# Performance work log

Hardware: AMD Instinct MI355X
Metric: run time of the kernel (lower is better)

The kernel has to match this reference:

```python
import jax, jax.numpy as jnp
import numpy as np

N, E, F_IN, H, C, G = 100000, 1600000, 128, 128, 10, 64


def setup_inputs() -> dict:
    key = jax.random.key(0)
    ks = jax.random.split(key, 9)
    x = jax.random.normal(ks[0], (N, F_IN), dtype=jnp.float32)
    edge_index = jax.random.randint(ks[1], (2, E), 0, N, dtype=jnp.int32)
    batch = jnp.sort(jax.random.randint(ks[2], (N,), 0, G, dtype=jnp.int32))
    s_in = 1.0 / np.sqrt(F_IN)
    s_h = 1.0 / np.sqrt(H)
    W1 = jax.random.normal(ks[3], (F_IN, H), jnp.float32) * s_in
    b1 = jnp.zeros((H,), jnp.float32)
    W2 = jax.random.normal(ks[4], (H, H), jnp.float32) * s_h
    b2 = jnp.zeros((H,), jnp.float32)
    Wfc = jax.random.normal(ks[5], (H, C), jnp.float32) * s_h
    bfc = jnp.zeros((C,), jnp.float32)
    return {"x": x, "edge_index": edge_index, "batch": batch,
            "W1": W1, "b1": b1, "W2": W2, "b2": b2, "Wfc": Wfc, "bfc": bfc}


def _gcn_conv(x, W, b, src, dst, n):
    # GCNConv: xW, symmetric deg^-1/2 normalization with self-loops, scatter-add, +bias
    xw = x @ W  # [N, H]
    deg = jnp.zeros((n,), xw.dtype).at[dst].add(1.0)  # in-degree incl. self-loop
    dis = jax.lax.rsqrt(jnp.maximum(deg, 1.0))
    norm = dis[src] * dis[dst]  # [E+N]
    out = jnp.zeros_like(xw).at[dst].add(xw[src] * norm[:, None])
    return out + b


def reference(x, edge_index, batch, W1, b1, W2, b2, Wfc, bfc):
    n = x.shape[0]
    loop = jnp.arange(n, dtype=edge_index.dtype)  # self-loops
    src = jnp.concatenate([edge_index[0], loop])
    dst = jnp.concatenate([edge_index[1], loop])
    h = jax.nn.relu(_gcn_conv(x, W1, b1, src, dst, n))
    h = jax.nn.relu(_gcn_conv(h, W2, b2, src, dst, n))
    # global mean pool over graph ids
    sums = jax.ops.segment_sum(h, batch, num_segments=G)  # [G, H]
    cnt = jax.ops.segment_sum(jnp.ones((n, 1), h.dtype), batch, num_segments=G)
    pooled = sums / jnp.maximum(cnt, 1.0)
    return pooled @ Wfc + bfc  # [G, C]
```

## Files before the change

kernel.cpp:

```cpp
#include <hip/hip_runtime.h>
#include <hip/hip_bf16.h>

#define NN 100000
#define NE 1600000
#define HD 128
#define NG 64
#define NC 10
#define NB 391
#define BCAP 4608
#define CHUNK 6400
#define NBIN (NE / CHUNK)

typedef short bf16x8 __attribute__((ext_vector_type(8)));
typedef float f32x4 __attribute__((ext_vector_type(4)));

__device__ __forceinline__ unsigned pk_bf16(float a, float b) {
  unsigned ua = __float_as_uint(a);
  unsigned ub = __float_as_uint(b);
  unsigned ra = (ua + 0x7fffu + ((ua >> 16) & 1u)) >> 16;
  unsigned rb = (ub + 0x7fffu + ((ub >> 16) & 1u)) >> 16;
  return ra | (rb << 16);
}

#define ACC_U4(v)                                  \
  do {                                             \
    a0 += __uint_as_float((v).x << 16);            \
    a1 += __uint_as_float((v).x & 0xffff0000u);    \
    a2 += __uint_as_float((v).y << 16);            \
    a3 += __uint_as_float((v).y & 0xffff0000u);    \
    a4 += __uint_as_float((v).z << 16);            \
    a5 += __uint_as_float((v).z & 0xffff0000u);    \
    a6 += __uint_as_float((v).w << 16);            \
    a7 += __uint_as_float((v).w & 0xffff0000u);    \
  } while (0)

__global__ __launch_bounds__(256) void k_bin2(const int* __restrict__ src, const int* __restrict__ dst,
                                              int* __restrict__ bcnt, unsigned* __restrict__ bkt,
                                              const float* __restrict__ W1, const float* __restrict__ W2,
                                              unsigned* __restrict__ WT1, unsigned* __restrict__ WT2,
                                              const int* __restrict__ bat, int* __restrict__ sg,
                                              int* __restrict__ eg, float* __restrict__ sums) {
  __shared__ int cl[NB];
  __shared__ int cb[NB];
  int bid = blockIdx.x;
  int tid = threadIdx.x;
  if (bid >= NBIN) {
    int mb = bid - NBIN;
    if (mb < 64) {
      int i = mb * 256 + tid;
      const float* W = (i < 8192) ? W1 : W2;
      unsigned* WT = (i < 8192) ? WT1 : WT2;
      int j = i & 8191;
      int n = j >> 6, kh = j & 63;
      WT[j] = pk_bf16(W[(2 * kh) * HD + n], W[(2 * kh + 1) * HD + n]);
      if (i < NG * HD) sums[i] = 0.f;
    } else {
      int i = (mb - 64) * 256 + tid;
      if (i < NN) {
        int g = bat[i];
        if (i == 0 || bat[i - 1] != g) sg[g] = i;
        if (i == NN - 1 || bat[i + 1] != g) eg[g] = i + 1;
      }
    }
    return;
  }
  int base_e = bid * CHUNK;
  for (int i = tid; i < NB; i += 256) cl[i] = 0;
  __syncthreads();
  #pragma unroll 5
  for (int j = 0; j < CHUNK / 256; ++j) {
    int d = dst[base_e + j * 256 + tid];
    atomicAdd(&cl[d >> 8], 1);
  }
  __syncthreads();
  for (int i = tid; i < NB; i += 256) {
    cb[i] = atomicAdd(&bcnt[i], cl[i]);
    cl[i] = 0;
  }
  __syncthreads();
  #pragma unroll 5
  for (int j = 0; j < CHUNK / 256; ++j) {
    int e = base_e + j * 256 + tid;
    int s = src[e];
    int d = dst[e];
    int b = d >> 8;
    int p = atomicAdd(&cl[b], 1);
    int idx = cb[b] + p;
    if (idx < BCAP)
      bkt[(size_t)b * BCAP + idx] = (unsigned)s | ((unsigned)(d & 255) << 24);
  }
}

__global__ __launch_bounds__(256) void k_fill2(const unsigned* __restrict__ bkt,
                                               const int* __restrict__ bcnt,
                                               int* __restrict__ rows, int* __restrict__ rowe,
                                               float* __restrict__ dis, int* __restrict__ csr) {
  __shared__ unsigned eds[BCAP];
  __shared__ int sc[256];
  int b = blockIdx.x;
  int tid = threadIdx.x;
  int n = bcnt[b];
  if (n > BCAP) n = BCAP;
  const unsigned* mb = bkt + (size_t)b * BCAP;
  for (int i = tid; i < n; i += 256) eds[i] = mb[i];
  sc[tid] = 0;
  __syncthreads();
  for (int i = tid; i < n; i += 256) atomicAdd(&sc[eds[i] >> 24], 1);
  __syncthreads();
  int deg = sc[tid];
  for (int off = 1; off < 256; off <<= 1) {
    int v = (tid >= off) ? sc[tid - off] : 0;
    __syncthreads();
    sc[tid] += v;
    __syncthreads();
  }
  int excl = sc[tid] - deg;
  int node = b * 256 + tid;
  int cbase = b * BCAP;
  if (node < NN) {
    rows[node] = cbase + excl;
    rowe[node] = cbase + excl + deg;
    dis[node] = rsqrtf((float)(deg + 1));
  }
  __syncthreads();
  sc[tid] = excl;
  __syncthreads();
  for (int i = tid; i < n; i += 256) {
    unsigned v = eds[i];
    int p = atomicAdd(&sc[v >> 24], 1);
    csr[cbase + p] = (int)(v & 0xFFFFFFu);
  }
}

template<bool BF16IN>
__global__ __launch_bounds__(256) void k_gemm_mfma(const void* __restrict__ Xin,
                                                   const unsigned* __restrict__ WT,
                                                   const float* __restrict__ dis,
                                                   unsigned* __restrict__ Y) {
  __shared__ char WL[128 * 256];
  __shared__ char XL[64 * 256];
  int t = threadIdx.x;
  int rowBase = blockIdx.x * 64;
  {
    const uint4* Wg = (const uint4*)WT;
    for (int i = t; i < 2048; i += 256) {
      int n = i >> 4, kq = i & 15;
      uint4 v = Wg[i];
      *(uint4*)(WL + ((n * 256 + kq * 16) ^ ((n & 7) << 4))) = v;
    }
  }
  if (BF16IN) {
    const uint4* Xg = (const uint4*)Xin;
    for (int i = t; i < 1024; i += 256) {
      int node = i >> 4, c = i & 15;
      int gn = rowBase + node; if (gn >= NN) gn = 0;
      uint4 v = Xg[(size_t)gn * 16 + c];
      *(uint4*)(XL + ((node * 256 + c * 16) ^ ((node & 7) << 4))) = v;
    }
  } else {
    const float4* Xg = (const float4*)Xin;
    for (int i = t; i < 1024; i += 256) {
      int node = i >> 4, c = i & 15;
      int gn = rowBase + node; if (gn >= NN) gn = 0;
      float4 a = Xg[(size_t)gn * 32 + c * 2];
      float4 b = Xg[(size_t)gn * 32 + c * 2 + 1];
      uint4 v;
      v.x = pk_bf16(a.x, a.y); v.y = pk_bf16(a.z, a.w);
      v.z = pk_bf16(b.x, b.y); v.w = pk_bf16(b.z, b.w);
      *(uint4*)(XL + ((node * 256 + c * 16) ^ ((node & 7) << 4))) = v;
    }
  }
  __syncthreads();
  int w = t >> 6, l = t & 63;
  int lr = l & 15, lh = l >> 4;
  int xnode = w * 16 + lr;
  bf16x8 bfrag[4];
  #pragma unroll
  for (int ks = 0; ks < 4; ++ks)
    bfrag[ks] = *(bf16x8*)(XL + ((xnode * 256 + (ks * 32 + lh * 8) * 2) ^ ((xnode & 7) << 4)));
  f32x4 acc[8];
  #pragma unroll
  for (int ct = 0; ct < 8; ++ct) acc[ct] = (f32x4){0.f, 0.f, 0.f, 0.f};
  #pragma unroll
  for (int ct = 0; ct < 8; ++ct) {
    int n = ct * 16 + lr;
    #pragma unroll
    for (int ks = 0; ks < 4; ++ks) {
      bf16x8 af = *(bf16x8*)(WL + ((n * 256 + (ks * 32 + lh * 8) * 2) ^ ((n & 7) << 4)));
      acc[ct] = __builtin_amdgcn_mfma_f32_16x16x32_bf16(af, bfrag[ks], acc[ct], 0, 0, 0);
    }
  }
  int gnode = rowBase + w * 16 + lr;
  if (gnode < NN) {
    float ds = dis[gnode];
    uint2* Yp = (uint2*)(Y + (size_t)gnode * 64);
    #pragma unroll
    for (int ct = 0; ct < 8; ++ct) {
      uint2 o;
      o.x = pk_bf16(acc[ct].x * ds, acc[ct].y * ds);
      o.y = pk_bf16(acc[ct].z * ds, acc[ct].w * ds);
      Yp[ct * 4 + lh] = o;
    }
  }
}

__global__ __launch_bounds__(256) void k_agg(const unsigned* __restrict__ Y, const int* __restrict__ rows,
                                             const int* __restrict__ rowe, const int* __restrict__ csr,
                                             const float* __restrict__ dis,
                                             const float* __restrict__ bias,
                                             unsigned* __restrict__ OUT) {
  int node = __builtin_amdgcn_readfirstlane((blockIdx.x << 2) + (threadIdx.x >> 6));
  int lane = threadIdx.x & 63;
  int sub = lane >> 4, li = lane & 15;
  const uint4* Yv = (const uint4*)Y;
  float a0 = 0.f, a1 = 0.f, a2 = 0.f, a3 = 0.f, a4 = 0.f, a5 = 0.f, a6 = 0.f, a7 = 0.f;
  int start = rows[node], len = rowe[node] - start;
  if (sub == 0) {
    uint4 sv = Yv[(size_t)node * 16 + li];
    ACC_U4(sv);
  }
  int i = start + ((len * sub) >> 2);
  int q1 = start + ((len * (sub + 1)) >> 2);
  for (; i + 4 <= q1; i += 4) {
    int s0 = csr[i], s1 = csr[i + 1], s2 = csr[i + 2], s3 = csr[i + 3];
    uint4 v0 = Yv[(size_t)s0 * 16 + li];
    uint4 v1 = Yv[(size_t)s1 * 16 + li];
    uint4 v2 = Yv[(size_t)s2 * 16 + li];
    uint4 v3 = Yv[(size_t)s3 * 16 + li];
    ACC_U4(v0);
    ACC_U4(v1);
    ACC_U4(v2);
    ACC_U4(v3);
  }
  for (; i < q1; ++i) {
    uint4 v = Yv[(size_t)csr[i] * 16 + li];
    ACC_U4(v);
  }
  a0 += __shfl_xor(a0, 16, 64); a0 += __shfl_xor(a0, 32, 64);
  a1 += __shfl_xor(a1, 16, 64); a1 += __shfl_xor(a1, 32, 64);
  a2 += __shfl_xor(a2, 16, 64); a2 += __shfl_xor(a2, 32, 64);
  a3 += __shfl_xor(a3, 16, 64); a3 += __shfl_xor(a3, 32, 64);
  a4 += __shfl_xor(a4, 16, 64); a4 += __shfl_xor(a4, 32, 64);
  a5 += __shfl_xor(a5, 16, 64); a5 += __shfl_xor(a5, 32, 64);
  a6 += __shfl_xor(a6, 16, 64); a6 += __shfl_xor(a6, 32, 64);
  a7 += __shfl_xor(a7, 16, 64); a7 += __shfl_xor(a7, 32, 64);
  if (sub != 0) return;
  float di = dis[node];
  const float4* bp = (const float4*)bias;
  float4 b0 = bp[li * 2], b1 = bp[li * 2 + 1];
  float o0 = fmaxf(fmaf(di, a0, b0.x), 0.f);
  float o1 = fmaxf(fmaf(di, a1, b0.y), 0.f);
  float o2 = fmaxf(fmaf(di, a2, b0.z), 0.f);
  float o3 = fmaxf(fmaf(di, a3, b0.w), 0.f);
  float o4 = fmaxf(fmaf(di, a4, b1.x), 0.f);
  float o5 = fmaxf(fmaf(di, a5, b1.y), 0.f);
  float o6 = fmaxf(fmaf(di, a6, b1.z), 0.f);
  float o7 = fmaxf(fmaf(di, a7, b1.w), 0.f);
  uint4 pv;
  pv.x = pk_bf16(o0, o1);
  pv.y = pk_bf16(o2, o3);
  pv.z = pk_bf16(o4, o5);
  pv.w = pk_bf16(o6, o7);
  ((uint4*)OUT)[(size_t)node * 16 + li] = pv;
}

__global__ __launch_bounds__(256) void k_pool(const unsigned* __restrict__ Hb, const int* __restrict__ sg,
                                              const int* __restrict__ eg, float* __restrict__ sums) {
  int g = blockIdx.x >> 3;
  int sl = blockIdx.x & 7;
  int slot = threadIdx.x >> 6;
  int pl = threadIdx.x & 63;
  int s = sg[g], e = eg[g];
  float f0 = 0.f, f1 = 0.f;
  for (int n = s + sl * 4 + slot; n < e; n += 32) {
    unsigned v = Hb[(size_t)n * 64 + pl];
    f0 += __uint_as_float(v << 16);
    f1 += __uint_as_float(v & 0xffff0000u);
  }
  atomicAdd(&sums[g * HD + 2 * pl], f0);
  atomicAdd(&sums[g * HD + 2 * pl + 1], f1);
}

__global__ __launch_bounds__(640) void k_fc(const float* __restrict__ sums, const int* __restrict__ sg,
                                            const int* __restrict__ eg, const float* __restrict__ Wfc,
                                            const float* __restrict__ bfc, float* __restrict__ out) {
  int t = threadIdx.x;
  if (t >= NG * NC) return;
  int g = t / NC, c = t - g * NC;
  int cntn = eg[g] - sg[g];
  float inv = 1.0f / fmaxf((float)cntn, 1.0f);
  float acc = 0.f;
  for (int f = 0; f < HD; ++f) acc = fmaf(sums[g * HD + f], Wfc[f * NC + c], acc);
  out[t] = acc * inv + bfc[c];
}

extern "C" void kernel_launch(void* const* d_in, const int* in_sizes, int n_in,
                              void* d_out, int out_size, void* d_ws, size_t ws_size,
                              hipStream_t stream) {
  const float* x   = (const float*)d_in[0];
  const int*   ei  = (const int*)d_in[1];
  const int*   bat = (const int*)d_in[2];
  const float* W1  = (const float*)d_in[3];
  const float* b1  = (const float*)d_in[4];
  const float* W2  = (const float*)d_in[5];
  const float* b2  = (const float*)d_in[6];
  const float* Wfc = (const float*)d_in[7];
  const float* bfc = (const float*)d_in[8];
  float* out = (float*)d_out;
  const int* esrc = ei;
  const int* edst = ei + NE;

  char* p = (char*)d_ws;
  auto carve = [&](size_t bytes) { char* r = p; p += (bytes + 255) & ~(size_t)255; return r; };
  float* dis  = (float*)carve((size_t)NN * 4);
  int*   rows = (int*)carve((size_t)NN * 4);
  int*   rowe = (int*)carve((size_t)NN * 4);
  int*   bcnt = (int*)carve((size_t)NB * 4);
  int*   sg   = (int*)carve(NG * 4);
  int*   eg   = (int*)carve(NG * 4);
  float* sums = (float*)carve(NG * HD * 4);
  unsigned* WT1 = (unsigned*)carve(8192 * 4);
  unsigned* WT2 = (unsigned*)carve(8192 * 4);
  int*   csr  = (int*)carve((size_t)NB * BCAP * 4);
  unsigned* Y   = (unsigned*)carve((size_t)NN * 64 * 4);
  unsigned* H1b = (unsigned*)carve((size_t)NN * 64 * 4);
  unsigned* bkt = Y;
  unsigned* H2b = H1b;

  hipMemsetAsync(bcnt, 0, (size_t)NB * 4, stream);

  int miscBlocks = 64 + (NN + 255) / 256;
  k_bin2<<<NBIN + miscBlocks, 256, 0, stream>>>(esrc, edst, bcnt, bkt,
                                                W1, W2, WT1, WT2, bat, sg, eg, sums);
  k_fill2<<<NB, 256, 0, stream>>>(bkt, bcnt, rows, rowe, dis, csr);

  int gblocks = (NN + 63) / 64;
  k_gemm_mfma<false><<<gblocks, 256, 0, stream>>>(x, WT1, dis, Y);
  k_agg<<<NN / 4, 256, 0, stream>>>(Y, rows, rowe, csr, dis, b1, H1b);
  k_gemm_mfma<true><<<gblocks, 256, 0, stream>>>(H1b, WT2, dis, Y);
  k_agg<<<NN / 4, 256, 0, stream>>>(Y, rows, rowe, csr, dis, b2, H2b);

  k_pool<<<NG * 8, 256, 0, stream>>>(H2b, sg, eg, sums);
  k_fc<<<1, 640, 0, stream>>>(sums, sg, eg, Wfc, bfc, out);
}
```

Baseline: 248.9 us.

## Cache dst in registers, use wave-shuffle scan, double pool parallelism

The binning kernel now keeps each thread's dst values in registers from the counting pass, so the second pass does not reload them from global memory. The fill kernel replaces a 256-step shared-memory Hillis-Steele scan, which needed many barriers, with a 64-lane shuffle scan plus a small cross-wave fixup. The pooling kernel launches twice as many blocks per graph, giving more parallelism at the cost of more atomics. These are small preprocessing and tail-kernel tweaks and leave the dominant GEMM and aggregation kernels unchanged.

```diff
diff --git a/kernel.cpp b/kernel.cpp
--- a/kernel.cpp
+++ b/kernel.cpp
@@ -10,6 +10,7 @@
 #define BCAP 4608
 #define CHUNK 6400
 #define NBIN (NE / CHUNK)
+#define EPT (CHUNK / 256)
 
 typedef short bf16x8 __attribute__((ext_vector_type(8)));
 typedef float f32x4 __attribute__((ext_vector_type(4)));
@@ -65,11 +66,13 @@
     return;
   }
   int base_e = bid * CHUNK;
+  int dc[EPT];
   for (int i = tid; i < NB; i += 256) cl[i] = 0;
   __syncthreads();
-  #pragma unroll 5
-  for (int j = 0; j < CHUNK / 256; ++j) {
+  #pragma unroll
+  for (int j = 0; j < EPT; ++j) {
     int d = dst[base_e + j * 256 + tid];
+    dc[j] = d;
     atomicAdd(&cl[d >> 8], 1);
   }
   __syncthreads();
@@ -78,11 +81,10 @@
     cl[i] = 0;
   }
   __syncthreads();
-  #pragma unroll 5
-  for (int j = 0; j < CHUNK / 256; ++j) {
-    int e = base_e + j * 256 + tid;
-    int s = src[e];
-    int d = dst[e];
+  #pragma unroll
+  for (int j = 0; j < EPT; ++j) {
+    int s = src[base_e + j * 256 + tid];
+    int d = dc[j];
     int b = d >> 8;
     int p = atomicAdd(&cl[b], 1);
     int idx = cb[b] + p;
@@ -97,6 +99,7 @@
                                                float* __restrict__ dis, int* __restrict__ csr) {
   __shared__ unsigned eds[BCAP];
   __shared__ int sc[256];
+  __shared__ int wsum[4];
   int b = blockIdx.x;
   int tid = threadIdx.x;
   int n = bcnt[b];
@@ -108,13 +111,19 @@
   for (int i = tid; i < n; i += 256) atomicAdd(&sc[eds[i] >> 24], 1);
   __syncthreads();
   int deg = sc[tid];
-  for (int off = 1; off < 256; off <<= 1) {
-    int v = (tid >= off) ? sc[tid - off] : 0;
-    __syncthreads();
-    sc[tid] += v;
-    __syncthreads();
-  }
-  int excl = sc[tid] - deg;
+  int v = deg;
+  int lane = tid & 63;
+  #pragma unroll
+  for (int off = 1; off < 64; off <<= 1) {
+    int u = __shfl_up(v, off, 64);
+    if (lane >= off) v += u;
+  }
+  if (lane == 63) wsum[tid >> 6] = v;
+  __syncthreads();
+  int base = 0;
+  #pragma unroll
+  for (int w = 0; w < 4; ++w) base += (w < (tid >> 6)) ? wsum[w] : 0;
+  int excl = base + v - deg;
   int node = b * 256 + tid;
   int cbase = b * BCAP;
   if (node < NN) {
@@ -126,9 +135,9 @@
   sc[tid] = excl;
   __syncthreads();
   for (int i = tid; i < n; i += 256) {
-    unsigned v = eds[i];
-    int p = atomicAdd(&sc[v >> 24], 1);
-    csr[cbase + p] = (int)(v & 0xFFFFFFu);
+    unsigned v2 = eds[i];
+    int p = atomicAdd(&sc[v2 >> 24], 1);
+    csr[cbase + p] = (int)(v2 & 0xFFFFFFu);
   }
 }
 
@@ -266,13 +275,13 @@
 
 __global__ __launch_bounds__(256) void k_pool(const unsigned* __restrict__ Hb, const int* __restrict__ sg,
                                               const int* __restrict__ eg, float* __restrict__ sums) {
-  int g = blockIdx.x >> 3;
-  int sl = blockIdx.x & 7;
+  int g = blockIdx.x >> 4;
+  int sl = blockIdx.x & 15;
   int slot = threadIdx.x >> 6;
   int pl = threadIdx.x & 63;
   int s = sg[g], e = eg[g];
   float f0 = 0.f, f1 = 0.f;
-  for (int n = s + sl * 4 + slot; n < e; n += 32) {
+  for (int n = s + sl * 4 + slot; n < e; n += 64) {
     unsigned v = Hb[(size_t)n * 64 + pl];
     f0 += __uint_as_float(v << 16);
     f1 += __uint_as_float(v & 0xffff0000u);
@@ -340,6 +349,6 @@
   k_gemm_mfma<true><<<gblocks, 256, 0, stream>>>(H1b, WT2, dis, Y);
   k_agg<<<NN / 4, 256, 0, stream>>>(Y, rows, rowe, csr, dis, b2, H2b);
 
-  k_pool<<<NG * 8, 256, 0, stream>>>(H2b, sg, eg, sums);
+  k_pool<<<NG * 16, 256, 0, stream>>>(H2b, sg, eg, sums);
   k_fc<<<1, 640, 0, stream>>>(sums, sg, eg, Wfc, bfc, out);
 }
```

Result: faster. 241.7 us (-2.9%).
